# Performance work log

Measured on AMD Instinct MI355X. Metric: run time of the kernel, lower is better.

Reference implementation:

```python
import jax, jax.numpy as jnp
import numpy as np

D_MODEL = 1024
NUM_HEADS = 16
D_FF = 4096
NEG_INF = -1e9


def _linear_params(key, d_in, d_out):
    kw, kb = jax.random.split(key)
    bound = 1.0 / np.sqrt(d_in)
    W = jax.random.uniform(kw, (d_in, d_out), jnp.float32, -bound, bound)
    b = jax.random.uniform(kb, (d_out,), jnp.float32, -bound, bound)
    return W, b


def setup_inputs() -> dict:
    key = jax.random.key(0)
    ks = jax.random.split(key, 8)
    B, S = 2, 2048
    x = jax.random.normal(ks[0], (B, S, D_MODEL), jnp.float32)
    # causal mask: 1 = attend, 0 = masked
    mask = jnp.tril(jnp.ones((S, S), jnp.bool_))[None, :, :]
    Wq, bq = _linear_params(ks[1], D_MODEL, D_MODEL)
    Wk, bk = _linear_params(ks[2], D_MODEL, D_MODEL)
    Wv, bv = _linear_params(ks[3], D_MODEL, D_MODEL)
    Wo, bo = _linear_params(ks[4], D_MODEL, D_MODEL)
    W1, b1 = _linear_params(ks[5], D_MODEL, D_FF)
    W2, b2 = _linear_params(ks[6], D_FF, D_MODEL)
    ln1_g = jnp.ones((D_MODEL,), jnp.float32)
    ln1_b = jnp.zeros((D_MODEL,), jnp.float32)
    ln2_g = jnp.ones((D_MODEL,), jnp.float32)
    ln2_b = jnp.zeros((D_MODEL,), jnp.float32)
    return {"x": x, "mask": mask,
            "Wq": Wq, "bq": bq, "Wk": Wk, "bk": bk, "Wv": Wv, "bv": bv,
            "Wo": Wo, "bo": bo, "W1": W1, "b1": b1, "W2": W2, "b2": b2,
            "ln1_g": ln1_g, "ln1_b": ln1_b, "ln2_g": ln2_g, "ln2_b": ln2_b}


def layer_norm(x, g, b, eps=1e-5):
    mu = jnp.mean(x, axis=-1, keepdims=True)
    var = jnp.mean(jnp.square(x - mu), axis=-1, keepdims=True)
    return (x - mu) * jax.lax.rsqrt(var + eps) * g + b


def attention(xn, mask, Wq, bq, Wk, bk, Wv, bv, Wo, bo):
    B, S, D = xn.shape
    H, dk = NUM_HEADS, D // NUM_HEADS
    q = (xn @ Wq + bq).reshape(B, S, H, dk).transpose(0, 2, 1, 3)  # [B,H,S,dk]
    k = (xn @ Wk + bk).reshape(B, S, H, dk).transpose(0, 2, 1, 3)
    v = (xn @ Wv + bv).reshape(B, S, H, dk).transpose(0, 2, 1, 3)
    scores = jnp.einsum("bhsd,bhtd->bhst", q, k) / jnp.sqrt(jnp.float32(dk))
    scores = jnp.where(mask[:, None, :, :], scores, NEG_INF)
    attn = jax.nn.softmax(scores, axis=-1)
    out = jnp.einsum("bhst,bhtd->bhsd", attn, v)  # [B,H,S,dk]
    out = out.transpose(0, 2, 1, 3).reshape(B, S, D)
    return out @ Wo + bo


def reference(x, mask, Wq, bq, Wk, bk, Wv, bv, Wo, bo, W1, b1, W2, b2,
              ln1_g, ln1_b, ln2_g, ln2_b):
    # pre-norm MHA + residual (dropout = identity at eval)
    h = x + attention(layer_norm(x, ln1_g, ln1_b), mask,
                      Wq, bq, Wk, bk, Wv, bv, Wo, bo)
    # pre-norm FFN + residual
    ff = jax.nn.relu(layer_norm(h, ln2_g, ln2_b) @ W1 + b1) @ W2 + b2
    return h + ff
```

## Files before the change

### kernel.cpp

```cpp
#include <hip/hip_runtime.h>

typedef unsigned short u16;
typedef __attribute__((ext_vector_type(8))) short    s16x8;
typedef __attribute__((ext_vector_type(8))) unsigned short u16x8;
typedef __attribute__((ext_vector_type(4))) float    f32x4;

typedef __attribute__((address_space(1))) const void gvoid_c;
typedef __attribute__((address_space(3))) void       lvoid;

__device__ __forceinline__ float b2f(u16 x) {
    return __builtin_bit_cast(float, (unsigned)x << 16);
}
__device__ __forceinline__ u16 f2bf(float f) {
    unsigned u = __builtin_bit_cast(unsigned, f);
    return (u16)((u + 0x7FFFu + ((u >> 16) & 1u)) >> 16);
}
__device__ __forceinline__ void gld16(const void* g, void* l) {
    __builtin_amdgcn_global_load_lds((gvoid_c*)g, (lvoid*)l, 16, 0, 0);
}

__global__ __launch_bounds__(256) void transpose_all(
    const float* __restrict__ Wq, const float* __restrict__ Wk,
    const float* __restrict__ Wv, const float* __restrict__ Wo,
    const float* __restrict__ W1, const float* __restrict__ W2,
    u16* __restrict__ Wqkv_t, u16* __restrict__ Wo_t,
    u16* __restrict__ W1_t, u16* __restrict__ W2_t)
{
    __shared__ u16 tile[32][33];
    int id = blockIdx.x;
    const float* src; u16* dst; int R, C, bx, by;
    if (id < 4096) {
        int m = id >> 10, r = id & 1023;
        bx = r & 31; by = r >> 5; R = 1024; C = 1024;
        src = (m == 0) ? Wq : (m == 1) ? Wk : (m == 2) ? Wv : Wo;
        dst = (m == 0) ? Wqkv_t : (m == 1) ? Wqkv_t + 1024 * 1024
            : (m == 2) ? Wqkv_t + 2048 * 1024 : Wo_t;
    } else if (id < 8192) {
        int r = id - 4096; bx = r & 127; by = r >> 7; R = 1024; C = 4096;
        src = W1; dst = W1_t;
    } else {
        int r = id - 8192; bx = r & 31; by = r >> 5; R = 4096; C = 1024;
        src = W2; dst = W2_t;
    }
    int tx = threadIdx.x & 31, ty = threadIdx.x >> 5;
    int c0 = bx * 32, r0 = by * 32;
#pragma unroll
    for (int i = 0; i < 32; i += 8)
        tile[ty + i][tx] = f2bf(src[(size_t)(r0 + ty + i) * C + c0 + tx]);
    __syncthreads();
#pragma unroll
    for (int i = 0; i < 32; i += 8)
        dst[(size_t)(c0 + ty + i) * R + r0 + tx] = tile[tx][ty + i];
}

__global__ void concat3(const float* a, const float* b, const float* c, float* o) {
    int i = blockIdx.x * blockDim.x + threadIdx.x;
    o[i] = (i < 1024) ? a[i] : (i < 2048 ? b[i - 1024] : c[i - 2048]);
}

__global__ __launch_bounds__(256) void ln_k(
    const float* __restrict__ in, const float* __restrict__ gg,
    const float* __restrict__ bb, u16* __restrict__ out)
{
    const int D = 1024;
    int row  = blockIdx.x * 4 + (threadIdx.x >> 6);
    int lane = threadIdx.x & 63;
    const float* ip = in + (size_t)row * D;
    float v[16];
#pragma unroll
    for (int cc = 0; cc < 4; cc++) {
        f32x4 t = *(const f32x4*)(ip + cc * 256 + lane * 4);
#pragma unroll
        for (int i = 0; i < 4; i++) v[cc * 4 + i] = t[i];
    }
    float s1 = 0.f, s2 = 0.f;
#pragma unroll
    for (int i = 0; i < 16; i++) { s1 += v[i]; s2 += v[i] * v[i]; }
#pragma unroll
    for (int m = 1; m < 64; m <<= 1) { s1 += __shfl_xor(s1, m); s2 += __shfl_xor(s2, m); }
    float mu   = s1 * (1.f / 1024.f);
    float var  = s2 * (1.f / 1024.f) - mu * mu;
    float rstd = rsqrtf(var + 1e-5f);
#pragma unroll
    for (int cc = 0; cc < 4; cc++) {
        int e = cc * 256 + lane * 4;
        f32x4 gv = *(const f32x4*)(gg + e);
        f32x4 bv = *(const f32x4*)(bb + e);
        u16 o[4];
#pragma unroll
        for (int i = 0; i < 4; i++)
            o[i] = f2bf((v[cc * 4 + i] - mu) * rstd * gv[i] + bv[i]);
        *(__attribute__((ext_vector_type(4))) unsigned short*)(out + (size_t)row * D + e) =
            (__attribute__((ext_vector_type(4))) unsigned short){o[0], o[1], o[2], o[3]};
    }
}

template <int BN, int RES, bool RELU, bool OUTF32>
__global__ __launch_bounds__(256) void gemm2(
    const u16* __restrict__ A, const u16* __restrict__ Bt,
    const float* __restrict__ bias, const float* __restrict__ res,
    void* __restrict__ out, int M, int N, int K)
{
    constexpr int NFR = BN / 32;
    __shared__ u16 As[2][4096];
    __shared__ u16 Bs[2][BN * 32];
    int tid = threadIdx.x, wave = tid >> 6, lane = tid & 63;
    int g = lane >> 4, c = lane & 15;
    int wm = wave >> 1, wn = wave & 1;

    int gx = gridDim.x, nwg = gx * gridDim.y;
    int id = blockIdx.y * gx + blockIdx.x;
    int swz = (id & 7) * (nwg >> 3) + (id >> 3);
    int m0 = (swz / gx) * 128, n0 = (swz % gx) * BN;

    f32x4 acc[4][NFR];
#pragma unroll
    for (int m = 0; m < 4; m++)
#pragma unroll
        for (int n = 0; n < NFR; n++) acc[m][n] = (f32x4){0, 0, 0, 0};

    int ch0 = wave * 128 + lane, ch1 = ch0 + 64;
    const u16* Ag0 = A + (size_t)(m0 + (ch0 >> 2)) * K + (ch0 & 3) * 8;
    const u16* Ag1 = A + (size_t)(m0 + (ch1 >> 2)) * K + (ch1 & 3) * 8;
    const u16* Bg0;
    const u16* Bg1 = nullptr;
    if constexpr (BN == 128) {
        Bg0 = Bt + (size_t)(n0 + (ch0 >> 2)) * K + (ch0 & 3) * 8;
        Bg1 = Bt + (size_t)(n0 + (ch1 >> 2)) * K + (ch1 & 3) * 8;
    } else {
        int chb = wave * 64 + lane;
        Bg0 = Bt + (size_t)(n0 + (chb >> 2)) * K + (chb & 3) * 8;
    }

    auto stage = [&](int buf, int kk) {
        gld16(Ag0 + kk, &As[buf][wave * 1024]);
        gld16(Ag1 + kk, &As[buf][wave * 1024 + 512]);
        if constexpr (BN == 128) {
            gld16(Bg0 + kk, &Bs[buf][wave * 1024]);
            gld16(Bg1 + kk, &Bs[buf][wave * 1024 + 512]);
        } else {
            gld16(Bg0 + kk, &Bs[buf][wave * 512]);
        }
    };

    int nt = K / 32;
    stage(0, 0);
    __syncthreads();
    int cur = 0;
    for (int t = 0; t < nt; t++) {
        if (t + 1 < nt) stage(cur ^ 1, (t + 1) * 32);
        s16x8 af[4], bfr[NFR];
#pragma unroll
        for (int m = 0; m < 4; m++)
            af[m] = *(const s16x8*)&As[cur][(wm * 64 + m * 16 + c) * 32 + g * 8];
#pragma unroll
        for (int n = 0; n < NFR; n++)
            bfr[n] = *(const s16x8*)&Bs[cur][(wn * (BN / 2) + n * 16 + c) * 32 + g * 8];
        __builtin_amdgcn_s_setprio(1);
#pragma unroll
        for (int m = 0; m < 4; m++)
#pragma unroll
            for (int n = 0; n < NFR; n++)
                acc[m][n] = __builtin_amdgcn_mfma_f32_16x16x32_bf16(af[m], bfr[n], acc[m][n], 0, 0, 0);
        __builtin_amdgcn_s_setprio(0);
        __syncthreads();
        cur ^= 1;
    }

#pragma unroll
    for (int n = 0; n < NFR; n++) {
        int col = n0 + wn * (BN / 2) + n * 16 + c;
        float bb = bias[col];
#pragma unroll
        for (int m = 0; m < 4; m++) {
#pragma unroll
            for (int j = 0; j < 4; j++) {
                int row = m0 + wm * 64 + m * 16 + g * 4 + j;
                float v = acc[m][n][j] + bb;
                if constexpr (RES == 2) v += res[(size_t)row * N + col];
                if constexpr (RELU) v = fmaxf(v, 0.f);
                if constexpr (OUTF32) ((float*)out)[(size_t)row * N + col] = v;
                else                  ((u16*)out)[(size_t)row * N + col] = f2bf(v);
            }
        }
    }
}

__global__ __launch_bounds__(256) void v_transpose(
    const u16* __restrict__ qkv, u16* __restrict__ vt)
{
    const int S = 2048, NC = 3072;
    __shared__ u16 tile[64][72];
    int st = blockIdx.x, bh = blockIdx.y, b = bh >> 4, h = bh & 15;
    int tid = threadIdx.x;
    int i = tid >> 3, cb8 = (tid & 7) * 8;
    const u16* src = qkv + (size_t)(b * S + st * 64) * NC + 2048 + h * 64;
    u16x8 a0 = *(const u16x8*)(src + (size_t)i * NC + cb8);
    u16x8 a1 = *(const u16x8*)(src + (size_t)(i + 32) * NC + cb8);
    *(u16x8*)&tile[i][cb8]      = a0;
    *(u16x8*)&tile[i + 32][cb8] = a1;
    __syncthreads();
    int d = tid >> 3, e8 = (tid & 7) * 8;
    int m = (d & 7) * 8;
#pragma unroll
    for (int rr = 0; rr < 2; rr++) {
        int r = d + rr * 32;
        u16x8 o;
#pragma unroll
        for (int j = 0; j < 8; j++) o[j] = tile[(e8 ^ m) + j][r];
        *(u16x8*)(vt + ((size_t)bh * 64 + r) * 2048 + st * 64 + e8) = o;
    }
}

__global__ __launch_bounds__(256) void attn_fwd3(
    const u16* __restrict__ qkv, const u16* __restrict__ vt,
    u16* __restrict__ o)
{
    const int S = 2048, NC = 3072;
    __shared__ u16 Ks[2][4096];
    __shared__ u16 Vs[2][4096];
    __shared__ u16 Plds[4][16][72];
    int qp = blockIdx.x, bh = blockIdx.y, b = bh >> 4, h = bh & 15;
    int tid = threadIdx.x, wave = tid >> 6, lane = tid & 63;
    int g = lane >> 4, c = lane & 15;
    int sr = tid >> 3, scb8 = (tid & 7) * 8;
    int mS = (sr & 7) * 8;
    int mR = (c & 7) * 8;

    const u16* kbase = qkv + (size_t)b * S * NC + 1024 + h * 64;
    const u16* vbase = vt + (size_t)bh * 64 * 2048;

    auto stageKV = [&](int buf, int t0) {
        gld16(kbase + (size_t)(t0 + sr)      * NC + (scb8 ^ mS), &Ks[buf][wave * 512]);
        gld16(kbase + (size_t)(t0 + sr + 32) * NC + (scb8 ^ mS), &Ks[buf][2048 + wave * 512]);
        gld16(vbase + (size_t)sr        * 2048 + t0 + scb8, &Vs[buf][wave * 512]);
        gld16(vbase + (size_t)(sr + 32) * 2048 + t0 + scb8, &Vs[buf][2048 + wave * 512]);
    };

#pragma unroll 1
    for (int ph = 0; ph < 2; ph++) {
        int qt = ph ? qp : 31 - qp;
        int q0 = qt * 64 + wave * 16;
        const u16* qptr = qkv + (size_t)(b * S + q0 + c) * NC + h * 64;
        s16x8 qf0 = *(const s16x8*)(qptr + g * 8);
        s16x8 qf1 = *(const s16x8*)(qptr + 32 + g * 8);

        float mr[4], lr[4];
        f32x4 acc[4];
#pragma unroll
        for (int j = 0; j < 4; j++) { mr[j] = -1e30f; lr[j] = 0.f; }
#pragma unroll
        for (int n = 0; n < 4; n++) acc[n] = (f32x4){0, 0, 0, 0};

        int ntiles = qt + 1;
        __syncthreads();
        stageKV(0, 0);
        __syncthreads();
        int cur = 0;
        for (int t = 0; t < ntiles; t++) {
            if (t + 1 < ntiles) stageKV(cur ^ 1, (t + 1) * 64);

            f32x4 s[4];
            __builtin_amdgcn_s_setprio(1);
#pragma unroll
            for (int kt = 0; kt < 4; kt++) {
                int r = kt * 16 + c;
                s16x8 kf0 = *(const s16x8*)&Ks[cur][r * 64 + ((g * 8) ^ mR)];
                s16x8 kf1 = *(const s16x8*)&Ks[cur][r * 64 + ((32 + g * 8) ^ mR)];
                f32x4 sv = (f32x4){0, 0, 0, 0};
                sv = __builtin_amdgcn_mfma_f32_16x16x32_bf16(qf0, kf0, sv, 0, 0, 0);
                sv = __builtin_amdgcn_mfma_f32_16x16x32_bf16(qf1, kf1, sv, 0, 0, 0);
                s[kt] = sv;
            }
            __builtin_amdgcn_s_setprio(0);
            int t0 = t * 64;
#pragma unroll
            for (int kt = 0; kt < 4; kt++) {
                int kcol = t0 + kt * 16 + c;
#pragma unroll
                for (int j = 0; j < 4; j++) {
                    int qrow = q0 + g * 4 + j;
                    s[kt][j] = (kcol <= qrow) ? s[kt][j] * 0.125f : -1e30f;
                }
            }
#pragma unroll
            for (int j = 0; j < 4; j++) {
                float tm = fmaxf(fmaxf(s[0][j], s[1][j]), fmaxf(s[2][j], s[3][j]));
#pragma unroll
                for (int m = 1; m < 16; m <<= 1) tm = fmaxf(tm, __shfl_xor(tm, m));
                float mnew = fmaxf(mr[j], tm);
                float corr = __expf(mr[j] - mnew);
                float rs = 0.f;
#pragma unroll
                for (int kt = 0; kt < 4; kt++) { float p = __expf(s[kt][j] - mnew); s[kt][j] = p; rs += p; }
#pragma unroll
                for (int m = 1; m < 16; m <<= 1) rs += __shfl_xor(rs, m);
                lr[j] = lr[j] * corr + rs;
                mr[j] = mnew;
#pragma unroll
                for (int n = 0; n < 4; n++) acc[n][j] *= corr;
            }
#pragma unroll
            for (int kt = 0; kt < 4; kt++)
#pragma unroll
                for (int j = 0; j < 4; j++)
                    Plds[wave][g * 4 + j][kt * 16 + c] = f2bf(s[kt][j]);
            s16x8 pa0 = *(const s16x8*)&Plds[wave][c][g * 8];
            s16x8 pa1 = *(const s16x8*)&Plds[wave][c][32 + g * 8];
            __builtin_amdgcn_s_setprio(1);
#pragma unroll
            for (int n = 0; n < 4; n++) {
                int r = n * 16 + c;
                s16x8 vb0 = *(const s16x8*)&Vs[cur][r * 64 + ((g * 8) ^ mR)];
                s16x8 vb1 = *(const s16x8*)&Vs[cur][r * 64 + ((32 + g * 8) ^ mR)];
                acc[n] = __builtin_amdgcn_mfma_f32_16x16x32_bf16(pa0, vb0, acc[n], 0, 0, 0);
                acc[n] = __builtin_amdgcn_mfma_f32_16x16x32_bf16(pa1, vb1, acc[n], 0, 0, 0);
            }
            __builtin_amdgcn_s_setprio(0);
            __syncthreads();
            cur ^= 1;
        }
#pragma unroll
        for (int j = 0; j < 4; j++) {
            float inv = 1.f / lr[j];
            size_t rbase = (size_t)(b * S + q0 + g * 4 + j) * 1024 + h * 64;
#pragma unroll
            for (int n = 0; n < 4; n++)
                o[rbase + n * 16 + c] = f2bf(acc[n][j] * inv);
        }
    }
}

extern "C" void kernel_launch(void* const* d_in, const int* in_sizes, int n_in,
                              void* d_out, int out_size, void* d_ws, size_t ws_size,
                              hipStream_t stream)
{
    const float* x    = (const float*)d_in[0];
    const float* Wq   = (const float*)d_in[2];  const float* bq = (const float*)d_in[3];
    const float* Wk   = (const float*)d_in[4];  const float* bk = (const float*)d_in[5];
    const float* Wv   = (const float*)d_in[6];  const float* bv = (const float*)d_in[7];
    const float* Wo   = (const float*)d_in[8];  const float* bo = (const float*)d_in[9];
    const float* W1   = (const float*)d_in[10]; const float* b1 = (const float*)d_in[11];
    const float* W2   = (const float*)d_in[12]; const float* b2 = (const float*)d_in[13];
    const float* ln1g = (const float*)d_in[14]; const float* ln1b = (const float*)d_in[15];
    const float* ln2g = (const float*)d_in[16]; const float* ln2b = (const float*)d_in[17];

    unsigned char* ws = (unsigned char*)d_ws;
    u16*   Wqkv_t = (u16*)(ws + 0);
    u16*   Wo_t   = (u16*)(ws + 6291456);
    u16*   W1_t   = (u16*)(ws + 8388608);
    u16*   W2_t   = (u16*)(ws + 16777216);
    float* bqkv   = (float*)(ws + 25165824);
    u16*   lnbuf  = (u16*)(ws + 25178112);
    u16*   qkvbuf = (u16*)(ws + 33566720);
    u16*   attnb  = (u16*)(ws + 58732544);
    u16*   f1buf  = (u16*)(ws + 33566720);
    float* hbuf   = (float*)(ws + 67121152);
    u16*   vtbuf  = (u16*)(ws + 67121152);

    transpose_all<<<12288, 256, 0, stream>>>(Wq, Wk, Wv, Wo, W1, W2,
                                             Wqkv_t, Wo_t, W1_t, W2_t);
    concat3<<<12, 256, 0, stream>>>(bq, bk, bv, bqkv);

    ln_k<<<1024, 256, 0, stream>>>(x, ln1g, ln1b, lnbuf);
    gemm2<128, 0, false, false><<<dim3(24, 32), 256, 0, stream>>>(
        lnbuf, Wqkv_t, bqkv, nullptr, qkvbuf, 4096, 3072, 1024);
    v_transpose<<<dim3(32, 32), 256, 0, stream>>>(qkvbuf, vtbuf);
    attn_fwd3<<<dim3(16, 32), 256, 0, stream>>>(qkvbuf, vtbuf, attnb);

    gemm2<64, 2, false, true><<<dim3(16, 32), 256, 0, stream>>>(
        attnb, Wo_t, bo, x, hbuf, 4096, 1024, 1024);

    ln_k<<<1024, 256, 0, stream>>>(hbuf, ln2g, ln2b, lnbuf);
    gemm2<128, 0, true, false><<<dim3(32, 32), 256, 0, stream>>>(
        lnbuf, W1_t, b1, nullptr, f1buf, 4096, 4096, 1024);
    gemm2<64, 2, false, true><<<dim3(16, 32), 256, 0, stream>>>(
        f1buf, W2_t, b2, hbuf, (float*)d_out, 4096, 1024, 4096);
}
```

Before: 412.6 us.

## Add K=64 N=64 GEMM, split masked attention tile, fold bias concat

```diff
diff --git a/kernel.cpp b/kernel.cpp
--- a/kernel.cpp
+++ b/kernel.cpp
@@ -15,6 +15,9 @@
     unsigned u = __builtin_bit_cast(unsigned, f);
     return (u16)((u + 0x7FFFu + ((u >> 16) & 1u)) >> 16);
 }
+__device__ __forceinline__ u16 f2bf_trunc(float f) {
+    return (u16)(__builtin_bit_cast(unsigned, f) >> 16);
+}
 __device__ __forceinline__ void gld16(const void* g, void* l) {
     __builtin_amdgcn_global_load_lds((gvoid_c*)g, (lvoid*)l, 16, 0, 0);
 }
@@ -23,11 +26,18 @@
     const float* __restrict__ Wq, const float* __restrict__ Wk,
     const float* __restrict__ Wv, const float* __restrict__ Wo,
     const float* __restrict__ W1, const float* __restrict__ W2,
+    const float* __restrict__ bq, const float* __restrict__ bk,
+    const float* __restrict__ bv,
     u16* __restrict__ Wqkv_t, u16* __restrict__ Wo_t,
-    u16* __restrict__ W1_t, u16* __restrict__ W2_t)
+    u16* __restrict__ W1_t, u16* __restrict__ W2_t, float* __restrict__ bqkv)
 {
     __shared__ u16 tile[32][33];
     int id = blockIdx.x;
+    if (id >= 12288) {
+        int i = (id - 12288) * 256 + threadIdx.x;
+        bqkv[i] = (i < 1024) ? bq[i] : (i < 2048 ? bk[i - 1024] : bv[i - 2048]);
+        return;
+    }
     const float* src; u16* dst; int R, C, bx, by;
     if (id < 4096) {
         int m = id >> 10, r = id & 1023;
@@ -53,11 +63,6 @@
         dst[(size_t)(c0 + ty + i) * R + r0 + tx] = tile[tx][ty + i];
 }
 
-__global__ void concat3(const float* a, const float* b, const float* c, float* o) {
-    int i = blockIdx.x * blockDim.x + threadIdx.x;
-    o[i] = (i < 1024) ? a[i] : (i < 2048 ? b[i - 1024] : c[i - 2048]);
-}
-
 __global__ __launch_bounds__(256) void ln_k(
     const float* __restrict__ in, const float* __restrict__ gg,
     const float* __restrict__ bb, u16* __restrict__ out)
@@ -181,6 +186,95 @@
                 if constexpr (RELU) v = fmaxf(v, 0.f);
                 if constexpr (OUTF32) ((float*)out)[(size_t)row * N + col] = v;
                 else                  ((u16*)out)[(size_t)row * N + col] = f2bf(v);
+            }
+        }
+    }
+}
+
+__global__ __launch_bounds__(256) void gemm_n64_k64(
+    const u16* __restrict__ A, const u16* __restrict__ Bt,
+    const float* __restrict__ bias, const float* __restrict__ res,
+    float* __restrict__ out, int M, int N, int K)
+{
+    __shared__ u16 As[2][8192];
+    __shared__ u16 Bs[2][4096];
+    int tid = threadIdx.x, wave = tid >> 6, lane = tid & 63;
+    int g = lane >> 4, c = lane & 15;
+    int wm = wave >> 1, wn = wave & 1;
+
+    int gx = gridDim.x, nwg = gx * gridDim.y;
+    int id = blockIdx.y * gx + blockIdx.x;
+    int swz = (id & 7) * (nwg >> 3) + (id >> 3);
+    int m0 = (swz / gx) * 128, n0 = (swz % gx) * 64;
+
+    f32x4 acc[4][2];
+#pragma unroll
+    for (int m = 0; m < 4; m++)
+#pragma unroll
+        for (int n = 0; n < 2; n++) acc[m][n] = (f32x4){0, 0, 0, 0};
+
+    const u16* asrc[4];
+#pragma unroll
+    for (int k = 0; k < 4; k++) {
+        int ch = k * 256 + tid, row = ch >> 3, c8 = ch & 7;
+        asrc[k] = A + (size_t)(m0 + row) * K + ((c8 ^ (row & 7)) * 8);
+    }
+    const u16* bsrc[2];
+#pragma unroll
+    for (int k = 0; k < 2; k++) {
+        int ch = k * 256 + tid, row = ch >> 3, c8 = ch & 7;
+        bsrc[k] = Bt + (size_t)(n0 + row) * K + ((c8 ^ (row & 7)) * 8);
+    }
+
+    auto stage = [&](int buf, int k0) {
+#pragma unroll
+        for (int k = 0; k < 4; k++)
+            gld16(asrc[k] + k0, &As[buf][(k * 256 + wave * 64) * 8]);
+#pragma unroll
+        for (int k = 0; k < 2; k++)
+            gld16(bsrc[k] + k0, &Bs[buf][(k * 256 + wave * 64) * 8]);
+    };
+
+    int nt = K / 64;
+    stage(0, 0);
+    __syncthreads();
+    int cur = 0;
+    int x7 = c & 7;
+    for (int t = 0; t < nt; t++) {
+        if (t + 1 < nt) stage(cur ^ 1, (t + 1) * 64);
+        s16x8 af[2][4], bfr[2][2];
+#pragma unroll
+        for (int kk = 0; kk < 2; kk++) {
+#pragma unroll
+            for (int m = 0; m < 4; m++)
+                af[kk][m] = *(const s16x8*)&As[cur][(wm * 64 + m * 16 + c) * 64 + ((kk * 4 + g) ^ x7) * 8];
+#pragma unroll
+            for (int n = 0; n < 2; n++)
+                bfr[kk][n] = *(const s16x8*)&Bs[cur][(wn * 32 + n * 16 + c) * 64 + ((kk * 4 + g) ^ x7) * 8];
+        }
+        __builtin_amdgcn_s_setprio(1);
+#pragma unroll
+        for (int kk = 0; kk < 2; kk++)
+#pragma unroll
+            for (int m = 0; m < 4; m++)
+#pragma unroll
+                for (int n = 0; n < 2; n++)
+                    acc[m][n] = __builtin_amdgcn_mfma_f32_16x16x32_bf16(af[kk][m], bfr[kk][n], acc[m][n], 0, 0, 0);
+        __builtin_amdgcn_s_setprio(0);
+        __syncthreads();
+        cur ^= 1;
+    }
+
+#pragma unroll
+    for (int n = 0; n < 2; n++) {
+        int col = n0 + wn * 32 + n * 16 + c;
+        float bb = bias[col];
+#pragma unroll
+        for (int m = 0; m < 4; m++) {
+#pragma unroll
+            for (int j = 0; j < 4; j++) {
+                int row = m0 + wm * 64 + m * 16 + g * 4 + j;
+                out[(size_t)row * N + col] = acc[m][n][j] + bb + res[(size_t)row * N + col];
             }
         }
     }
@@ -212,7 +306,7 @@
     }
 }
 
-__global__ __launch_bounds__(256) void attn_fwd3(
+__global__ __launch_bounds__(256) void attn_fwd4(
     const u16* __restrict__ qkv, const u16* __restrict__ vt,
     u16* __restrict__ o)
 {
@@ -252,14 +346,7 @@
 #pragma unroll
         for (int n = 0; n < 4; n++) acc[n] = (f32x4){0, 0, 0, 0};
 
-        int ntiles = qt + 1;
-        __syncthreads();
-        stageKV(0, 0);
-        __syncthreads();
-        int cur = 0;
-        for (int t = 0; t < ntiles; t++) {
-            if (t + 1 < ntiles) stageKV(cur ^ 1, (t + 1) * 64);
-
+        auto do_tile = [&](int cur, int t0, bool masked) __attribute__((always_inline)) {
             f32x4 s[4];
             __builtin_amdgcn_s_setprio(1);
 #pragma unroll
@@ -273,14 +360,17 @@
                 s[kt] = sv;
             }
             __builtin_amdgcn_s_setprio(0);
-            int t0 = t * 64;
 #pragma unroll
             for (int kt = 0; kt < 4; kt++) {
-                int kcol = t0 + kt * 16 + c;
 #pragma unroll
                 for (int j = 0; j < 4; j++) {
-                    int qrow = q0 + g * 4 + j;
-                    s[kt][j] = (kcol <= qrow) ? s[kt][j] * 0.125f : -1e30f;
+                    if (masked) {
+                        int kcol = t0 + kt * 16 + c;
+                        int qrow = q0 + g * 4 + j;
+                        s[kt][j] = (kcol <= qrow) ? s[kt][j] * 0.125f : -1e30f;
+                    } else {
+                        s[kt][j] *= 0.125f;
+                    }
                 }
             }
 #pragma unroll
@@ -304,7 +394,7 @@
             for (int kt = 0; kt < 4; kt++)
 #pragma unroll
                 for (int j = 0; j < 4; j++)
-                    Plds[wave][g * 4 + j][kt * 16 + c] = f2bf(s[kt][j]);
+                    Plds[wave][g * 4 + j][kt * 16 + c] = f2bf_trunc(s[kt][j]);
             s16x8 pa0 = *(const s16x8*)&Plds[wave][c][g * 8];
             s16x8 pa1 = *(const s16x8*)&Plds[wave][c][32 + g * 8];
             __builtin_amdgcn_s_setprio(1);
@@ -317,9 +407,20 @@
                 acc[n] = __builtin_amdgcn_mfma_f32_16x16x32_bf16(pa1, vb1, acc[n], 0, 0, 0);
             }
             __builtin_amdgcn_s_setprio(0);
+        };
+
+        __syncthreads();
+        stageKV(0, 0);
+        __syncthreads();
+        int cur = 0;
+        for (int t = 0; t < qt; t++) {
+            stageKV(cur ^ 1, (t + 1) * 64);
+            do_tile(cur, t * 64, false);
             __syncthreads();
             cur ^= 1;
         }
+        do_tile(cur, qt * 64, true);
+
 #pragma unroll
         for (int j = 0; j < 4; j++) {
             float inv = 1.f / lr[j];
@@ -358,22 +459,21 @@
     float* hbuf   = (float*)(ws + 67121152);
     u16*   vtbuf  = (u16*)(ws + 67121152);
 
-    transpose_all<<<12288, 256, 0, stream>>>(Wq, Wk, Wv, Wo, W1, W2,
-                                             Wqkv_t, Wo_t, W1_t, W2_t);
-    concat3<<<12, 256, 0, stream>>>(bq, bk, bv, bqkv);
+    transpose_all<<<12300, 256, 0, stream>>>(Wq, Wk, Wv, Wo, W1, W2, bq, bk, bv,
+                                             Wqkv_t, Wo_t, W1_t, W2_t, bqkv);
 
     ln_k<<<1024, 256, 0, stream>>>(x, ln1g, ln1b, lnbuf);
     gemm2<128, 0, false, false><<<dim3(24, 32), 256, 0, stream>>>(
         lnbuf, Wqkv_t, bqkv, nullptr, qkvbuf, 4096, 3072, 1024);
     v_transpose<<<dim3(32, 32), 256, 0, stream>>>(qkvbuf, vtbuf);
-    attn_fwd3<<<dim3(16, 32), 256, 0, stream>>>(qkvbuf, vtbuf, attnb);
-
-    gemm2<64, 2, false, true><<<dim3(16, 32), 256, 0, stream>>>(
+    attn_fwd4<<<dim3(16, 32), 256, 0, stream>>>(qkvbuf, vtbuf, attnb);
+
+    gemm_n64_k64<<<dim3(16, 32), 256, 0, stream>>>(
         attnb, Wo_t, bo, x, hbuf, 4096, 1024, 1024);
 
     ln_k<<<1024, 256, 0, stream>>>(hbuf, ln2g, ln2b, lnbuf);
     gemm2<128, 0, true, false><<<dim3(32, 32), 256, 0, stream>>>(
         lnbuf, W1_t, b1, nullptr, f1buf, 4096, 4096, 1024);
-    gemm2<64, 2, false, true><<<dim3(16, 32), 256, 0, stream>>>(
+    gemm_n64_k64<<<dim3(16, 32), 256, 0, stream>>>(
         f1buf, W2_t, b2, hbuf, (float*)d_out, 4096, 1024, 4096);
 }
```

Measured after the change: 382.0 us. 1.08x faster.
